# Kernel optimization log

Measured on AMD Instinct MI355X. Metric: run time of the kernel, lower is better.

The kernel has to match this reference:

```python
import jax, jax.numpy as jnp
import numpy as np

B, L, D, H, K_DELAYS = 8, 2048, 512, 8, 8
DH = D // H


def setup_inputs() -> dict:
    key = jax.random.key(0)
    ks = jax.random.split(key, 6)
    def lin_w(k):
        return 0.02 * jax.random.normal(k, (D, D), jnp.float32)
    return {
        "x_q":  jax.random.normal(ks[0], (B, L, D), jnp.float32),
        "x_kv": jax.random.normal(ks[1], (B, L, D), jnp.float32),
        "Wq": lin_w(ks[2]), "bq": jnp.zeros((D,), jnp.float32),
        "Wk": lin_w(ks[3]), "bk": jnp.zeros((D,), jnp.float32),
        "Wv": lin_w(ks[4]), "bv": jnp.zeros((D,), jnp.float32),
        "Wo": lin_w(ks[5]), "bo": jnp.zeros((D,), jnp.float32),
    }


def reference(x_q, x_kv, Wq, bq, Wk, bk, Wv, bv, Wo, bo):
    Bx, Lx, Dx = x_q.shape

    def proj(x, W, b):  # torch Linear: x @ W.T + b, then split heads -> [B,H,L,dh]
        return (x @ W.T + b).reshape(Bx, Lx, H, DH).transpose(0, 2, 1, 3)

    q = proj(x_q, Wq, bq)
    k = proj(x_kv, Wk, bk)
    v = proj(x_kv, Wv, bv)

    # FFT-based autocorrelation over the time axis (axis=2)
    qz = q - q.mean(axis=2, keepdims=True)
    kz = k - k.mean(axis=2, keepdims=True)
    Qf = jnp.fft.rfft(qz, axis=2)
    Kf = jnp.fft.rfft(kz, axis=2)
    corr = jnp.fft.irfft(Qf * jnp.conj(Kf), n=Lx, axis=2).mean(axis=-1)  # [B,H,L]
    # torch expands corr to [B,H,Lq,Lk] then means over Lq -> identical to corr
    score = corr

    K = min(K_DELAYS, Lx)
    vals, idx = jax.lax.top_k(score, K)                    # [B,H,K]
    w = vals / (vals.sum(axis=-1, keepdims=True) + 1e-12)
    w = jax.lax.stop_gradient(w)                           # .detach() in torch

    # circular shift by -delay == gather at (t + delay) mod L
    t = jnp.arange(Lx)
    pos = (t[None, None, None, :] + idx[..., None]) % Lx   # [B,H,K,L]
    v_sh = jnp.take_along_axis(v[:, :, None, :, :], pos[..., None], axis=3)  # [B,H,K,L,dh]
    out = jnp.einsum('bhk,bhkld->bhld', w, v_sh)           # weighted sum over delays

    out = out.transpose(0, 2, 1, 3).reshape(Bx, Lx, Dx)
    return out @ Wo.T + bo
```

## Files before the change

kernel.cpp:

```cpp
#include <hip/hip_runtime.h>
#include <math.h>

#define BB 8
#define LL 2048
#define DD 512
#define HH 8
#define DHH 64
#define KD 8
#define MM (BB*LL)

typedef _Float16 f16x2 __attribute__((ext_vector_type(2)));
typedef _Float16 f16x4 __attribute__((ext_vector_type(4)));
typedef _Float16 f16x8 __attribute__((ext_vector_type(8)));
typedef float    f32x4 __attribute__((ext_vector_type(4)));

__device__ inline void cvt8(const float* __restrict__ s, _Float16* hp, _Float16* lp) {
    const float4 a = *(const float4*)s;
    const float4 b = *(const float4*)(s + 4);
    const float v[8] = {a.x, a.y, a.z, a.w, b.x, b.y, b.z, b.w};
    f16x8 hi, lo;
#pragma unroll
    for (int j = 0; j < 8; j++) {
        const _Float16 h = (_Float16)v[j];
        hi[j] = h;
        lo[j] = (_Float16)((v[j] - (float)h) * 512.0f);
    }
    *(f16x8*)hp = hi;
    if (lp) *(f16x8*)lp = lo;
}

__global__ __launch_bounds__(256) void prep_all(const float* __restrict__ xq,
                                                const float* __restrict__ xkv,
                                                const float* __restrict__ Wq, const float* __restrict__ Wk,
                                                const float* __restrict__ Wv, const float* __restrict__ Wo,
                                                _Float16* __restrict__ Xq_h, _Float16* __restrict__ Xq_l,
                                                _Float16* __restrict__ Xkv_h, _Float16* __restrict__ Xkv_l,
                                                _Float16* __restrict__ Wq_h, _Float16* __restrict__ Wq_l,
                                                _Float16* __restrict__ Wk_h, _Float16* __restrict__ Wk_l,
                                                _Float16* __restrict__ Wv_h, _Float16* __restrict__ Wo_h) {
    const int bid = blockIdx.x;
    if (bid < 8192) {
        const int g = bid * 256 + threadIdx.x;
        const int which = g >> 20;
        const size_t idx = (size_t)(g & 1048575) * 8;
        const float* src = which ? xkv : xq;
        _Float16* dh = which ? Xkv_h : Xq_h;
        _Float16* dl = which ? Xkv_l : Xq_l;
        cvt8(src + idx, dh + idx, dl + idx);
    } else {
        const int g = (bid - 8192) * 256 + threadIdx.x;
        const int which = g >> 15;
        const size_t idx = (size_t)(g & 32767) * 8;
        if (which == 0)      cvt8(Wq + idx, Wq_h + idx, Wq_l + idx);
        else if (which == 1) cvt8(Wk + idx, Wk_h + idx, Wk_l + idx);
        else if (which == 2) cvt8(Wv + idx, Wv_h + idx, nullptr);
        else                 cvt8(Wo + idx, Wo_h + idx, nullptr);
    }
}

template<int NPROD, int MODE>
__device__ __forceinline__ void gemm_body(const _Float16* __restrict__ Ag,
                                          const _Float16* __restrict__ Al_g,
                                          const _Float16* __restrict__ Bg,
                                          const _Float16* __restrict__ Bl_g,
                                          const float* __restrict__ bias,
                                          void* __restrict__ Cv,
                                          _Float16* lds, int l0) {
    _Float16* Ah = lds;
    _Float16* Bh = lds + 5120;
    _Float16* Al = (NPROD == 3) ? lds + 10240 : lds;
    _Float16* Bl = (NPROD == 3) ? lds + 15360 : lds;

    const int t  = threadIdx.x;
    const int m0 = (((l0 >> 5) << 3) | (l0 & 7)) * 128;
    const int n0 = ((l0 >> 3) & 3) * 128;

    const int lrow = t >> 2;
    const int lcol = (t & 3) * 8;
    const int wave = t >> 6;
    const int lane = t & 63;
    const int wm   = (wave >> 1) * 64;
    const int wn   = (wave & 1) * 64;
    const int lm   = lane & 15;
    const int quad = lane >> 4;

    f32x4 acc0[4][4] = {};
    f32x4 acc1[4][4] = {};

    f16x8 pa[2], pb[2], pal[2], pbl[2];
#pragma unroll
    for (int p = 0; p < 2; p++) {
        pa[p] = *(const f16x8*)(Ag + (size_t)(m0 + p * 64 + lrow) * 512 + lcol);
        pb[p] = *(const f16x8*)(Bg + (size_t)(n0 + p * 64 + lrow) * 512 + lcol);
        if (NPROD == 3) {
            pal[p] = *(const f16x8*)(Al_g + (size_t)(m0 + p * 64 + lrow) * 512 + lcol);
            pbl[p] = *(const f16x8*)(Bl_g + (size_t)(n0 + p * 64 + lrow) * 512 + lcol);
        }
    }

    for (int k0 = 0; k0 < 512; k0 += 32) {
        __syncthreads();
#pragma unroll
        for (int p = 0; p < 2; p++) {
            const int row = p * 64 + lrow;
            *(f16x8*)&Ah[row * 40 + lcol] = pa[p];
            *(f16x8*)&Bh[row * 40 + lcol] = pb[p];
            if (NPROD == 3) {
                *(f16x8*)&Al[row * 40 + lcol] = pal[p];
                *(f16x8*)&Bl[row * 40 + lcol] = pbl[p];
            }
        }
        __syncthreads();

        if (k0 + 32 < 512) {
            const int kn = k0 + 32;
#pragma unroll
            for (int p = 0; p < 2; p++) {
                pa[p] = *(const f16x8*)(Ag + (size_t)(m0 + p * 64 + lrow) * 512 + kn + lcol);
                pb[p] = *(const f16x8*)(Bg + (size_t)(n0 + p * 64 + lrow) * 512 + kn + lcol);
                if (NPROD == 3) {
                    pal[p] = *(const f16x8*)(Al_g + (size_t)(m0 + p * 64 + lrow) * 512 + kn + lcol);
                    pbl[p] = *(const f16x8*)(Bl_g + (size_t)(n0 + p * 64 + lrow) * 512 + kn + lcol);
                }
            }
        }

        f16x8 afh[4], bf[4];
#pragma unroll
        for (int mt = 0; mt < 4; mt++)
            afh[mt] = *(f16x8*)&Ah[(wm + mt * 16 + lm) * 40 + quad * 8];
#pragma unroll
        for (int nt = 0; nt < 4; nt++)
            bf[nt] = *(f16x8*)&Bh[(wn + nt * 16 + lm) * 40 + quad * 8];

#pragma unroll
        for (int mt = 0; mt < 4; mt++)
#pragma unroll
            for (int nt = 0; nt < 4; nt++)
                acc0[mt][nt] = __builtin_amdgcn_mfma_f32_16x16x32_f16(afh[mt], bf[nt], acc0[mt][nt], 0, 0, 0);

        if (NPROD == 3) {
            f16x8 afl[4];
#pragma unroll
            for (int mt = 0; mt < 4; mt++)
                afl[mt] = *(f16x8*)&Al[(wm + mt * 16 + lm) * 40 + quad * 8];
#pragma unroll
            for (int mt = 0; mt < 4; mt++)
#pragma unroll
                for (int nt = 0; nt < 4; nt++)
                    acc1[mt][nt] = __builtin_amdgcn_mfma_f32_16x16x32_f16(afl[mt], bf[nt], acc1[mt][nt], 0, 0, 0);
#pragma unroll
            for (int nt = 0; nt < 4; nt++)
                bf[nt] = *(f16x8*)&Bl[(wn + nt * 16 + lm) * 40 + quad * 8];
#pragma unroll
            for (int mt = 0; mt < 4; mt++)
#pragma unroll
                for (int nt = 0; nt < 4; nt++)
                    acc1[mt][nt] = __builtin_amdgcn_mfma_f32_16x16x32_f16(afh[mt], bf[nt], acc1[mt][nt], 0, 0, 0);
        }
    }

#pragma unroll
    for (int mt = 0; mt < 4; mt++) {
#pragma unroll
        for (int nt = 0; nt < 4; nt++) {
            const int n = n0 + wn + nt * 16 + lm;
            const float bv = bias[n];
            float val[4];
#pragma unroll
            for (int r = 0; r < 4; r++) {
                val[r] = acc0[mt][nt][r] + bv;
                if (NPROD == 3) val[r] += acc1[mt][nt][r] * (1.0f / 512.0f);
            }
            const int mbase = m0 + wm + mt * 16 + quad * 4;
            const int b_idx = mbase >> 11;
            const int lbase = mbase & 2047;
            if (MODE == 0) {
                float* C = (float*)Cv;
#pragma unroll
                for (int r = 0; r < 4; r++) C[(size_t)(mbase + r) * 512 + n] = val[r];
            } else if (MODE == 1) {
                float* C = (float*)Cv;
                float4 pv = make_float4(val[0], val[1], val[2], val[3]);
                *(float4*)&C[((size_t)(b_idx * 512 + n)) * 2048 + lbase] = pv;
            } else {
                _Float16* C = (_Float16*)Cv;
#pragma unroll
                for (int r = 0; r < 4; r++)
                    C[(size_t)b_idx * 1048576 + (size_t)(n >> 6) * 131072
                      + (size_t)(lbase + r) * 64 + (n & 63)] = (_Float16)val[r];
            }
        }
    }
}

__global__ __launch_bounds__(256, 2) void gemm_qk(const _Float16* __restrict__ A0h, const _Float16* __restrict__ A0l,
                                                  const _Float16* __restrict__ B0h, const _Float16* __restrict__ B0l,
                                                  const float* __restrict__ bias0, float* __restrict__ C0,
                                                  const _Float16* __restrict__ A1h, const _Float16* __restrict__ A1l,
                                                  const _Float16* __restrict__ B1h, const _Float16* __restrict__ B1l,
                                                  const float* __restrict__ bias1, float* __restrict__ C1) {
    __shared__ __align__(16) _Float16 lds[20480];
    const int prob = blockIdx.x >> 9;
    const int l0   = blockIdx.x & 511;
    if (prob == 0)
        gemm_body<3, 1>(A0h, A0l, B0h, B0l, bias0, C0, lds, l0);
    else
        gemm_body<3, 1>(A1h, A1l, B1h, B1l, bias1, C1, lds, l0);
}

__global__ __launch_bounds__(256, 2) void gemm_v(const _Float16* __restrict__ Ah_g,
                                                 const _Float16* __restrict__ Bh_g,
                                                 const float* __restrict__ bias,
                                                 _Float16* __restrict__ C) {
    __shared__ __align__(16) _Float16 lds[10240];
    gemm_body<1, 2>(Ah_g, Ah_g, Bh_g, Bh_g, bias, C, lds, blockIdx.x);
}

__global__ __launch_bounds__(256, 2) void gemm_o(const _Float16* __restrict__ Ah_g,
                                                 const _Float16* __restrict__ Bh_g,
                                                 const float* __restrict__ bias,
                                                 float* __restrict__ C) {
    __shared__ __align__(16) _Float16 lds[10240];
    gemm_body<1, 0>(Ah_g, Ah_g, Bh_g, Bh_g, bias, C, lds, blockIdx.x);
}

#define PAD3(i) ((i) + ((i) >> 3))

__device__ inline float2 cmul2(float2 a, float2 w) {
    return make_float2(a.x * w.x - a.y * w.y, a.x * w.y + a.y * w.x);
}
__device__ inline float2 cadd2(float2 a, float2 b) { return make_float2(a.x + b.x, a.y + b.y); }
__device__ inline float2 csub2(float2 a, float2 b) { return make_float2(a.x - b.x, a.y - b.y); }

__global__ __launch_bounds__(256) void fft_fwd(const float* __restrict__ qT,
                                               const float* __restrict__ kT,
                                               float* __restrict__ specP) {
    const int blk  = blockIdx.x;
    const int bh   = blk >> 4;
    const int part = blk & 15;
    const int t    = threadIdx.x;
    __shared__ float2 Zs[2304];
    __shared__ float2 Wt[1024];

#pragma unroll
    for (int s = 0; s < 4; s++) {
        const int j = t + s * 256;
        float sv, cv;
        __sincosf(2.0f * (float)M_PI * (float)j / 2048.0f, &sv, &cv);
        Wt[j] = make_float2(cv, -sv);
    }

    float2 pacc[8];
#pragma unroll
    for (int s = 0; s < 8; s++) pacc[s] = make_float2(0.0f, 0.0f);

    const int low5 = t & 31, hi3 = t >> 5;
    const int low2 = t & 3,  hi6 = t >> 2;

    for (int j4 = 0; j4 < 4; j4++) {
        const int seq = bh * 64 + part * 4 + j4;
        const float* qp = qT + (size_t)seq * 2048;
        const float* kp = kT + (size_t)seq * 2048;
        float2 z[8];
#pragma unroll
        for (int s = 0; s < 8; s++) z[s] = make_float2(qp[t + 256 * s], kp[t + 256 * s]);
        __syncthreads();

#pragma unroll
        for (int sp = 0; sp < 4; sp++) {
            float2 u = z[sp], v = z[sp + 4];
            z[sp]     = cadd2(u, v);
            z[sp + 4] = cmul2(csub2(u, v), Wt[t + 256 * sp]);
        }
#pragma unroll
        for (int base = 0; base < 8; base += 4)
#pragma unroll
            for (int q2 = 0; q2 < 2; q2++) {
                float2 u = z[base + q2], v = z[base + q2 + 2];
                z[base + q2]     = cadd2(u, v);
                z[base + q2 + 2] = cmul2(csub2(u, v), Wt[2 * (t + 256 * q2)]);
            }
        {
            const float2 w = Wt[4 * t];
#pragma unroll
            for (int e = 0; e < 8; e += 2) {
                float2 u = z[e], v = z[e + 1];
                z[e]     = cadd2(u, v);
                z[e + 1] = cmul2(csub2(u, v), w);
            }
        }

#pragma unroll
        for (int s = 0; s < 8; s++) Zs[PAD3(t + 256 * s)] = z[s];
        __syncthreads();
#pragma unroll
        for (int s = 0; s < 8; s++) z[s] = Zs[PAD3(low5 + 32 * s + 256 * hi3)];

#pragma unroll
        for (int sp = 0; sp < 4; sp++) {
            float2 u = z[sp], v = z[sp + 4];
            z[sp]     = cadd2(u, v);
            z[sp + 4] = cmul2(csub2(u, v), Wt[8 * (low5 + 32 * sp)]);
        }
#pragma unroll
        for (int base = 0; base < 8; base += 4)
#pragma unroll
            for (int q2 = 0; q2 < 2; q2++) {
                float2 u = z[base + q2], v = z[base + q2 + 2];
                z[base + q2]     = cadd2(u, v);
                z[base + q2 + 2] = cmul2(csub2(u, v), Wt[16 * (low5 + 32 * q2)]);
            }
        {
            const float2 w = Wt[32 * low5];
#pragma unroll
            for (int e = 0; e < 8; e += 2) {
                float2 u = z[e], v = z[e + 1];
                z[e]     = cadd2(u, v);
                z[e + 1] = cmul2(csub2(u, v), w);
            }
        }

#pragma unroll
        for (int s = 0; s < 8; s++) Zs[PAD3(low5 + 32 * s + 256 * hi3)] = z[s];
        __syncthreads();
#pragma unroll
        for (int s = 0; s < 8; s++) z[s] = Zs[PAD3(low2 + 4 * s + 32 * hi6)];

#pragma unroll
        for (int sp = 0; sp < 4; sp++) {
            float2 u = z[sp], v = z[sp + 4];
            z[sp]     = cadd2(u, v);
            z[sp + 4] = cmul2(csub2(u, v), Wt[64 * (low2 + 4 * sp)]);
        }
#pragma unroll
        for (int base = 0; base < 8; base += 4)
#pragma unroll
            for (int q2 = 0; q2 < 2; q2++) {
                float2 u = z[base + q2], v = z[base + q2 + 2];
                z[base + q2]     = cadd2(u, v);
                z[base + q2 + 2] = cmul2(csub2(u, v), Wt[128 * (low2 + 4 * q2)]);
            }
        {
            const float2 w = Wt[256 * low2];
#pragma unroll
            for (int e = 0; e < 8; e += 2) {
                float2 u = z[e], v = z[e + 1];
                z[e]     = cadd2(u, v);
                z[e + 1] = cmul2(csub2(u, v), w);
            }
        }

#pragma unroll
        for (int s = 0; s < 8; s++) Zs[PAD3(low2 + 4 * s + 32 * hi6)] = z[s];
        __syncthreads();
#pragma unroll
        for (int s = 0; s < 8; s++) z[s] = Zs[PAD3(8 * t + s)];

#pragma unroll
        for (int base = 0; base < 8; base += 4) {
            {
                float2 u = z[base], v = z[base + 2];
                z[base]     = cadd2(u, v);
                z[base + 2] = csub2(u, v);
            }
            {
                float2 u = z[base + 1], v = z[base + 3];
                float2 d = csub2(u, v);
                z[base + 1] = cadd2(u, v);
                z[base + 3] = make_float2(d.y, -d.x);
            }
        }
#pragma unroll
        for (int e = 0; e < 8; e += 2) {
            float2 u = z[e], v = z[e + 1];
            z[e]     = cadd2(u, v);
            z[e + 1] = csub2(u, v);
        }

#pragma unroll
        for (int s = 0; s < 8; s++) Zs[PAD3(8 * t + s)] = z[s];
        __syncthreads();

#pragma unroll
        for (int s = 0; s < 8; s++) {
            const int p  = t + 256 * s;
            const int f  = (int)(__brev((unsigned)p) >> 21);
            const int fm = (2048 - f) & 2047;
            const int p2 = (int)(__brev((unsigned)fm) >> 21);
            const float2 zf = Zs[PAD3(p)];
            const float2 zm = Zs[PAD3(p2)];
            const float qr = 0.5f * (zf.x + zm.x);
            const float qi = 0.5f * (zf.y - zm.y);
            const float kr = 0.5f * (zf.y + zm.y);
            const float ki = 0.5f * (zm.x - zf.x);
            if (f != 0) {
                pacc[s].x += qr * kr + qi * ki;
                pacc[s].y += qi * kr - qr * ki;
            }
        }
    }

    float2* outp = (float2*)specP + (size_t)blk * 2048;
#pragma unroll
    for (int s = 0; s < 8; s++) outp[t + 256 * s] = pacc[s];
}

__device__ inline void build_twiddle(float2* Wt, int tid, float sign) {
#pragma unroll
    for (int s = 0; s < 4; s++) {
        const int j = tid + s * 256;
        const float a = 2.0f * (float)M_PI * (float)j / 2048.0f;
        float sv, cv;
        __sincosf(a, &sv, &cv);
        Wt[j] = make_float2(cv, sign * sv);
    }
}

__device__ inline void fft2048_stages(float2* Z, const float2* Wt, int tid) {
    for (int st = 0; st < 11; st++) {
        const int half = 1 << st;
        const int shift = 10 - st;
#pragma unroll
        for (int r = 0; r < 4; r++) {
            const int m   = tid + r * 256;
            const int grp = m >> st;
            const int pos = m & (half - 1);
            const int i0  = (grp << (st + 1)) + pos;
            const int i1  = i0 + half;
            const float2 w = Wt[pos << shift];
            const float2 a = Z[i0];
            const float2 b = Z[i1];
            const float tr = b.x * w.x - b.y * w.y;
            const float ti = b.x * w.y + b.y * w.x;
            Z[i0] = make_float2(a.x + tr, a.y + ti);
            Z[i1] = make_float2(a.x - tr, a.y - ti);
        }
        __syncthreads();
    }
}

__global__ __launch_bounds__(256) void fft_inv_topk(const float* __restrict__ specP,
                                                    int* __restrict__ delays,
                                                    float* __restrict__ weights) {
    const int bh  = blockIdx.x;
    const int tid = threadIdx.x;
    __shared__ float2 Z[2048];
    __shared__ float2 Wt[1024];
    __shared__ float  corrS[2048];
    __shared__ float  rv[256];
    __shared__ int    ri[256];
    __shared__ float  vals[KD];
    __shared__ int    inds[KD];

    build_twiddle(Wt, tid, +1.0f);

    const float2* sp = (const float2*)specP + (size_t)bh * 16 * 2048;
#pragma unroll
    for (int s = 0; s < 8; s++) {
        const int p = tid + s * 256;
        float2 acc = make_float2(0.0f, 0.0f);
#pragma unroll
        for (int part = 0; part < 16; part++) {
            const float2 v = sp[part * 2048 + p];
            acc.x += v.x; acc.y += v.y;
        }
        Z[p] = acc;
    }
    __syncthreads();
    fft2048_stages(Z, Wt, tid);

    const float scale = 1.0f / (2048.0f * 64.0f);
#pragma unroll
    for (int s = 0; s < 8; s++) {
        const int i = tid + s * 256;
        corrS[i] = Z[i].x * scale;
    }
    __syncthreads();

    for (int k = 0; k < KD; k++) {
        float best = -1e30f;
        int   bi   = 1 << 30;
        for (int i = tid; i < 2048; i += 256) {
            const float v = corrS[i];
            if (v > best || (v == best && i < bi)) { best = v; bi = i; }
        }
        rv[tid] = best;
        ri[tid] = bi;
        __syncthreads();
        for (int off = 128; off > 0; off >>= 1) {
            if (tid < off) {
                const float v2 = rv[tid + off];
                const int   i2 = ri[tid + off];
                if (v2 > rv[tid] || (v2 == rv[tid] && i2 < ri[tid])) {
                    rv[tid] = v2; ri[tid] = i2;
                }
            }
            __syncthreads();
        }
        if (tid == 0) {
            vals[k] = rv[0];
            inds[k] = ri[0];
            corrS[ri[0]] = -1e30f;
        }
        __syncthreads();
    }

    if (tid == 0) {
        float sum = 0.0f;
        for (int k = 0; k < KD; k++) sum += vals[k];
        const float inv = 1.0f / (sum + 1e-12f);
        for (int k = 0; k < KD; k++) {
            weights[bh * KD + k] = vals[k] * inv;
            delays[bh * KD + k]  = inds[k];
        }
    }
}

__global__ __launch_bounds__(256) void gather_ws(const _Float16* __restrict__ v,
                                                 const int* __restrict__ delays,
                                                 const float* __restrict__ weights,
                                                 _Float16* __restrict__ outb) {
    const int gp = blockIdx.x * 256 + threadIdx.x;
    const int c8 = gp & 63;
    const int m  = gp >> 6;
    const int l  = m & 2047;
    const int b  = m >> 11;
    const int ch = c8 * 8;
    const int h  = ch >> 6;
    const int dh = ch & 63;
    const int bh = b * 8 + h;

    const _Float16* vb = v + (size_t)bh * 131072;
    float a[8] = {};
#pragma unroll
    for (int k = 0; k < KD; k++) {
        const int   d = delays[bh * KD + k];
        const float w = weights[bh * KD + k];
        const int   p = (l + d) & 2047;
        const f16x8 pv = *(const f16x8*)&vb[p * 64 + dh];
#pragma unroll
        for (int j = 0; j < 8; j++) a[j] = fmaf(w, (float)pv[j], a[j]);
    }
    f16x8 ov;
#pragma unroll
    for (int j = 0; j < 8; j++) ov[j] = (_Float16)a[j];
    *(f16x8*)&outb[(size_t)m * 512 + ch] = ov;
}

extern "C" void kernel_launch(void* const* d_in, const int* in_sizes, int n_in,
                              void* d_out, int out_size, void* d_ws, size_t ws_size,
                              hipStream_t stream) {
    const float* x_q  = (const float*)d_in[0];
    const float* x_kv = (const float*)d_in[1];
    const float* Wq   = (const float*)d_in[2];
    const float* bq   = (const float*)d_in[3];
    const float* Wk   = (const float*)d_in[4];
    const float* bk   = (const float*)d_in[5];
    const float* Wv   = (const float*)d_in[6];
    const float* bv   = (const float*)d_in[7];
    const float* Wo   = (const float*)d_in[8];
    const float* bo   = (const float*)d_in[9];
    float* out = (float*)d_out;

    char* ws = (char*)d_ws;
    _Float16* Xq_h  = (_Float16*)(ws + 0);
    _Float16* Xq_l  = (_Float16*)(ws + 16777216);
    _Float16* Xkv_h = (_Float16*)(ws + 33554432);
    _Float16* Xkv_l = (_Float16*)(ws + 50331648);
    _Float16* Wq_h  = (_Float16*)(ws + 67108864);
    _Float16* Wq_l  = (_Float16*)(ws + 67633152);
    _Float16* Wk_h  = (_Float16*)(ws + 68157440);
    _Float16* Wk_l  = (_Float16*)(ws + 68681728);
    _Float16* Wv_h  = (_Float16*)(ws + 69206016);
    _Float16* Wo_h  = (_Float16*)(ws + 69730304);
    int*      dely  = (int*)    (ws + 70254592);
    float*    wgt   = (float*)  (ws + 70256640);
    float*    kf32  = (float*)  (ws + 75497472);
    float*    specP = (float*)  (ws + 50331648);
    _Float16* vh    = (_Float16*)(ws + 0);
    _Float16* gbuf  = (_Float16*)(ws + 16777216);
    float*    qf32  = (float*)d_out;

    (void)0;

    dim3 blk(256);

    prep_all<<<dim3(8704), blk, 0, stream>>>(x_q, x_kv, Wq, Wk, Wv, Wo,
                                             Xq_h, Xq_l, Xkv_h, Xkv_l,
                                             Wq_h, Wq_l, Wk_h, Wk_l, Wv_h, Wo_h);

    gemm_qk<<<dim3(512), blk, 0, stream>>>(Xq_h, Xq_l, Wq_h, Wq_l, bq, qf32,
                                           Xq_h, Xq_l, Wq_h, Wq_l, bq, qf32);
    {
        float* kf32_ = (float*)(ws + 0);
        gemm_qk<<<dim3(512), blk, 0, stream>>>(Xkv_h, Xkv_l, Wk_h, Wk_l, bk, kf32_,
                                               Xkv_h, Xkv_l, Wk_h, Wk_l, bk, kf32_);
    }

    fft_fwd<<<dim3(1024), blk, 0, stream>>>(qf32, (float*)(ws + 0), specP);
    fft_inv_topk<<<dim3(BB * HH), blk, 0, stream>>>(specP, dely, wgt);

    gemm_v<<<dim3(512), blk, 0, stream>>>(Xkv_h, Wv_h, bv, vh);

    gather_ws<<<dim3(4096), blk, 0, stream>>>(vh, dely, wgt, gbuf);

    gemm_o<<<dim3(512), blk, 0, stream>>>(gbuf, Wo_h, bo, out);
}
```

Baseline: 294.8 us.

## Merge Q/K projections into one launch and co-schedule inverse FFT with V GEMM

The Q and K projection GEMMs now run as a single 1024-block launch instead of two 512-block launches. The 64-block inverse-FFT/top-k kernel is merged with the V projection GEMM into one grid, so the small, poorly occupied top-k stage overlaps GEMM work. Workspace buffers are moved to separate offsets so K, spectra, V and the gather output no longer alias. This removes launch gaps and tail underutilization, at the cost of a larger shared-memory allocation for the GEMM blocks.

```diff
diff --git a/kernel.cpp b/kernel.cpp
--- a/kernel.cpp
+++ b/kernel.cpp
@@ -9,7 +9,6 @@
 #define KD 8
 #define MM (BB*LL)
 
-typedef _Float16 f16x2 __attribute__((ext_vector_type(2)));
 typedef _Float16 f16x4 __attribute__((ext_vector_type(4)));
 typedef _Float16 f16x8 __attribute__((ext_vector_type(8)));
 typedef float    f32x4 __attribute__((ext_vector_type(4)));
@@ -209,14 +208,6 @@
         gemm_body<3, 1>(A1h, A1l, B1h, B1l, bias1, C1, lds, l0);
 }
 
-__global__ __launch_bounds__(256, 2) void gemm_v(const _Float16* __restrict__ Ah_g,
-                                                 const _Float16* __restrict__ Bh_g,
-                                                 const float* __restrict__ bias,
-                                                 _Float16* __restrict__ C) {
-    __shared__ __align__(16) _Float16 lds[10240];
-    gemm_body<1, 2>(Ah_g, Ah_g, Bh_g, Bh_g, bias, C, lds, blockIdx.x);
-}
-
 __global__ __launch_bounds__(256, 2) void gemm_o(const _Float16* __restrict__ Ah_g,
                                                  const _Float16* __restrict__ Bh_g,
                                                  const float* __restrict__ bias,
@@ -406,17 +397,6 @@
     for (int s = 0; s < 8; s++) outp[t + 256 * s] = pacc[s];
 }
 
-__device__ inline void build_twiddle(float2* Wt, int tid, float sign) {
-#pragma unroll
-    for (int s = 0; s < 4; s++) {
-        const int j = tid + s * 256;
-        const float a = 2.0f * (float)M_PI * (float)j / 2048.0f;
-        float sv, cv;
-        __sincosf(a, &sv, &cv);
-        Wt[j] = make_float2(cv, sign * sv);
-    }
-}
-
 __device__ inline void fft2048_stages(float2* Z, const float2* Wt, int tid) {
     for (int st = 0; st < 11; st++) {
         const int half = 1 << st;
@@ -440,20 +420,26 @@
     }
 }
 
-__global__ __launch_bounds__(256) void fft_inv_topk(const float* __restrict__ specP,
-                                                    int* __restrict__ delays,
-                                                    float* __restrict__ weights) {
-    const int bh  = blockIdx.x;
+__device__ void inv_topk_body(const float* __restrict__ specP,
+                              int* __restrict__ delays,
+                              float* __restrict__ weights,
+                              char* smem, int bh) {
     const int tid = threadIdx.x;
-    __shared__ float2 Z[2048];
-    __shared__ float2 Wt[1024];
-    __shared__ float  corrS[2048];
-    __shared__ float  rv[256];
-    __shared__ int    ri[256];
-    __shared__ float  vals[KD];
-    __shared__ int    inds[KD];
-
-    build_twiddle(Wt, tid, +1.0f);
+    float2* Z     = (float2*)smem;
+    float2* Wt    = Z + 2048;
+    float*  corrS = (float*)(Wt + 1024);
+    float*  rv    = corrS + 2048;
+    int*    ri    = (int*)(rv + 256);
+    float*  vals  = (float*)(ri + 256);
+    int*    inds  = (int*)(vals + KD);
+
+#pragma unroll
+    for (int s = 0; s < 4; s++) {
+        const int j = tid + s * 256;
+        float sv, cv;
+        __sincosf(2.0f * (float)M_PI * (float)j / 2048.0f, &sv, &cv);
+        Wt[j] = make_float2(cv, sv);
+    }
 
     const float2* sp = (const float2*)specP + (size_t)bh * 16 * 2048;
 #pragma unroll
@@ -515,6 +501,20 @@
             delays[bh * KD + k]  = inds[k];
         }
     }
+}
+
+__global__ __launch_bounds__(256, 2) void inv_and_v(const float* __restrict__ specP,
+                                                    int* __restrict__ delays,
+                                                    float* __restrict__ weights,
+                                                    const _Float16* __restrict__ Xkv_h,
+                                                    const _Float16* __restrict__ Wv_h,
+                                                    const float* __restrict__ bv,
+                                                    _Float16* __restrict__ vh) {
+    __shared__ __align__(16) char smem[34880];
+    if (blockIdx.x < 512)
+        gemm_body<1, 2>(Xkv_h, Xkv_h, Wv_h, Wv_h, bv, vh, (_Float16*)smem, blockIdx.x);
+    else
+        inv_topk_body(specP, delays, weights, smem, blockIdx.x - 512);
 }
 
 __global__ __launch_bounds__(256) void gather_ws(const _Float16* __restrict__ v,
@@ -577,12 +577,10 @@
     int*      dely  = (int*)    (ws + 70254592);
     float*    wgt   = (float*)  (ws + 70256640);
     float*    kf32  = (float*)  (ws + 75497472);
-    float*    specP = (float*)  (ws + 50331648);
-    _Float16* vh    = (_Float16*)(ws + 0);
-    _Float16* gbuf  = (_Float16*)(ws + 16777216);
+    float*    specP = (float*)  (ws + 113246208);
+    _Float16* vh    = (_Float16*)(ws + 130023424);
+    _Float16* gbuf  = (_Float16*)(ws + 146800640);
     float*    qf32  = (float*)d_out;
-
-    (void)0;
 
     dim3 blk(256);
 
@@ -590,18 +588,12 @@
                                              Xq_h, Xq_l, Xkv_h, Xkv_l,
                                              Wq_h, Wq_l, Wk_h, Wk_l, Wv_h, Wo_h);
 
-    gemm_qk<<<dim3(512), blk, 0, stream>>>(Xq_h, Xq_l, Wq_h, Wq_l, bq, qf32,
-                                           Xq_h, Xq_l, Wq_h, Wq_l, bq, qf32);
-    {
-        float* kf32_ = (float*)(ws + 0);
-        gemm_qk<<<dim3(512), blk, 0, stream>>>(Xkv_h, Xkv_l, Wk_h, Wk_l, bk, kf32_,
-                                               Xkv_h, Xkv_l, Wk_h, Wk_l, bk, kf32_);
-    }
-
-    fft_fwd<<<dim3(1024), blk, 0, stream>>>(qf32, (float*)(ws + 0), specP);
-    fft_inv_topk<<<dim3(BB * HH), blk, 0, stream>>>(specP, dely, wgt);
-
-    gemm_v<<<dim3(512), blk, 0, stream>>>(Xkv_h, Wv_h, bv, vh);
+    gemm_qk<<<dim3(1024), blk, 0, stream>>>(Xq_h,  Xq_l,  Wq_h, Wq_l, bq, qf32,
+                                            Xkv_h, Xkv_l, Wk_h, Wk_l, bk, kf32);
+
+    fft_fwd<<<dim3(1024), blk, 0, stream>>>(qf32, kf32, specP);
+
+    inv_and_v<<<dim3(576), blk, 0, stream>>>(specP, dely, wgt, Xkv_h, Wv_h, bv, vh);
 
     gather_ws<<<dim3(4096), blk, 0, stream>>>(vh, dely, wgt, gbuf);
 
```

Result: slower. 307.5 us (+4.3%).
